# Kernel optimization log

Hardware: AMD Instinct MI355X
Metric: run time of the kernel (lower is better)

Reference implementation:

```python
import jax, jax.numpy as jnp
import numpy as np

B, C, H, W = 4, 256, 64, 64
G = 32          # GroupNorm groups
EPS = 1e-6


def setup_inputs() -> dict:
    key = jax.random.key(0)
    ks = jax.random.split(key, 6)
    inp = {
        "x": jax.random.normal(ks[0], (B, C, H, W), dtype=jnp.float32),
        "gamma": jnp.ones((C,), jnp.float32),
        "beta": jnp.zeros((C,), jnp.float32),
        "wq": jax.random.normal(ks[1], (C, C), jnp.float32) * 0.02,
        "bq": jnp.zeros((C,), jnp.float32),
        "wk": jax.random.normal(ks[2], (C, C), jnp.float32) * 0.02,
        "bk": jnp.zeros((C,), jnp.float32),
        "wv": jax.random.normal(ks[3], (C, C), jnp.float32) * 0.02,
        "bv": jnp.zeros((C,), jnp.float32),
        "wp": jax.random.normal(ks[4], (C, C), jnp.float32) * 0.02,
        "bp": jnp.zeros((C,), jnp.float32),
    }
    return inp


def _group_norm(x, gamma, beta):
    b, c, h, w = x.shape
    xs = x.reshape(b, G, c // G, h, w)
    mu = xs.mean(axis=(2, 3, 4), keepdims=True)
    var = xs.var(axis=(2, 3, 4), keepdims=True)  # biased, matches torch GroupNorm
    xn = ((xs - mu) * jax.lax.rsqrt(var + EPS)).reshape(b, c, h, w)
    return xn * gamma[None, :, None, None] + beta[None, :, None, None]


def _conv1x1(s, w, bias):
    # 1x1 conv == per-pixel channel matmul
    return jnp.einsum('oc,bchw->bohw', w, s) + bias[None, :, None, None]


def reference(x, gamma, beta, wq, bq, wk, bk, wv, bv, wp, bp):
    b, c, h, w = x.shape
    s = _group_norm(x, gamma, beta)
    q = _conv1x1(s, wq, bq).reshape(b, c, h * w)  # [B, C, N]
    k = _conv1x1(s, wk, bk).reshape(b, c, h * w)
    v = _conv1x1(s, wv, bv).reshape(b, c, h * w)
    # scores[b,i,j] = sum_c q[b,c,i] k[b,c,j], scaled by C^-1/2
    scores = jnp.einsum('bci,bcj->bij', q, k) * (c ** -0.5)
    attn = jax.nn.softmax(scores, axis=2)
    # h_[b,c,i] = sum_j v[b,c,j] attn[b,i,j]
    h_ = jnp.einsum('bij,bcj->bci', attn, v).reshape(b, c, h, w)
    h_ = _conv1x1(h_, wp, bp)
    return x + h_
```

## Files before the change

kernel.cpp:

```cpp
#include <hip/hip_runtime.h>

#define BB 4
#define CCH 256
#define NPIX 4096
#define EPS 1e-6f

typedef __attribute__((ext_vector_type(8))) short bf16x8;
typedef __attribute__((ext_vector_type(4))) float f32x4;
typedef __attribute__((ext_vector_type(16))) float f32x16;

__device__ __forceinline__ unsigned short f2bf(float f) {
    return (unsigned short)((__float_as_uint(f) + 0x8000u) >> 16);
}
__device__ __forceinline__ float bf2f(unsigned short h) {
    return __uint_as_float((unsigned)h << 16);
}
__device__ __forceinline__ void gl2lds16(const void* g, void* l) {
    __builtin_amdgcn_global_load_lds(
        (const __attribute__((address_space(1))) unsigned int*)g,
        (__attribute__((address_space(3))) unsigned int*)l, 16, 0, 0);
}

__global__ __launch_bounds__(256) void gn_apply(const float* __restrict__ x,
                                                const float* __restrict__ gamma,
                                                const float* __restrict__ beta,
                                                unsigned short* __restrict__ sb) {
    int bg = blockIdx.x;
    int b = bg >> 5, g = bg & 31;
    const float4* x4 = (const float4*)(x + (size_t)(b * CCH + g * 8) * NPIX);
    float s = 0.f, ss = 0.f;
    for (int e = threadIdx.x; e < 8 * NPIX / 4; e += 256) {
        float4 v = x4[e];
        s += v.x + v.y + v.z + v.w;
        ss += v.x * v.x + v.y * v.y + v.z * v.z + v.w * v.w;
    }
    __shared__ float rs[256], rss[256];
    __shared__ float mean_s, rstd_s;
    rs[threadIdx.x] = s; rss[threadIdx.x] = ss;
    __syncthreads();
    for (int off = 128; off > 0; off >>= 1) {
        if (threadIdx.x < (unsigned)off) {
            rs[threadIdx.x] += rs[threadIdx.x + off];
            rss[threadIdx.x] += rss[threadIdx.x + off];
        }
        __syncthreads();
    }
    if (threadIdx.x == 0) {
        const float inv = 1.0f / (float)(8 * NPIX);
        float m = rs[0] * inv;
        float var = rss[0] * inv - m * m;
        mean_s = m;
        rstd_s = rsqrtf(var + EPS);
    }
    __syncthreads();
    float scale[8], shift[8];
#pragma unroll
    for (int ci = 0; ci < 8; ++ci) {
        float ga = gamma[g * 8 + ci], be = beta[g * 8 + ci];
        scale[ci] = rstd_s * ga;
        shift[ci] = be - mean_s * scale[ci];
    }
#pragma unroll 1
    for (int r = 0; r < 4; ++r) {
        int pq = r * 256 + threadIdx.x;
        __align__(16) unsigned short h[4][8];
#pragma unroll
        for (int ci = 0; ci < 8; ++ci) {
            float4 v = x4[ci * 1024 + pq];
            h[0][ci] = f2bf(v.x * scale[ci] + shift[ci]);
            h[1][ci] = f2bf(v.y * scale[ci] + shift[ci]);
            h[2][ci] = f2bf(v.z * scale[ci] + shift[ci]);
            h[3][ci] = f2bf(v.w * scale[ci] + shift[ci]);
        }
        size_t base = ((size_t)(b * NPIX + pq * 4) << 8) + g * 8;
#pragma unroll
        for (int p = 0; p < 4; ++p)
            *(uint4*)(sb + base + (size_t)p * 256) = *(const uint4*)h[p];
    }
}

__global__ __launch_bounds__(256) void wcvt(const float* __restrict__ wq,
                                            const float* __restrict__ wk,
                                            const float* __restrict__ wv,
                                            const float* __restrict__ wp,
                                            unsigned short* __restrict__ wb) {
    int e = blockIdx.x * 256 + threadIdx.x;
    const float* srcs[4] = {wp, wq, wk, wv};
#pragma unroll
    for (int m = 0; m < 4; ++m) {
        float4 v = ((const float4*)srcs[m])[e];
        ushort4 h;
        h.x = f2bf(v.x); h.y = f2bf(v.y); h.z = f2bf(v.z); h.w = f2bf(v.w);
        *(ushort4*)(wb + (size_t)m * 65536 + (size_t)e * 4) = h;
    }
}

__global__ __launch_bounds__(256) void qkv_mfma(
    const unsigned short* __restrict__ sb, const unsigned short* __restrict__ wb,
    const float* __restrict__ bq, const float* __restrict__ bk,
    const float* __restrict__ bv,
    unsigned short* __restrict__ qT, unsigned short* __restrict__ kT,
    unsigned short* __restrict__ vB) {
    __shared__ __align__(16) char lds[34816];
    const int tid = threadIdx.x, lane = tid & 63, w = tid >> 6;
    const int ln15 = lane & 15, q = lane >> 4;
    const int n0 = blockIdx.x * 128;
    const int co0 = blockIdx.y * 128;
    const int z = blockIdx.z;
    const unsigned short* wm = wb + (size_t)(z + 1) * 65536;
    const float* bias = (z == 0) ? bq : (z == 1) ? bk : bv;

    f32x4 acc[2][8];
#pragma unroll
    for (int i2 = 0; i2 < 2; ++i2)
#pragma unroll
        for (int nf = 0; nf < 8; ++nf) {
            acc[i2][nf][0] = 0.f; acc[i2][nf][1] = 0.f;
            acc[i2][nf][2] = 0.f; acc[i2][nf][3] = 0.f;
        }

#pragma unroll 1
    for (int kt = 0; kt < 4; ++kt) {
#pragma unroll
        for (int r = 0; r < 4; ++r) {
            int gch = r * 256 + tid;
            int row = gch >> 3, sidx = gch & 7;
            int cc = sidx ^ (row & 7);
            gl2lds16(sb + ((size_t)(n0 + row) << 8) + kt * 64 + cc * 8,
                     &lds[r * 4096 + w * 1024]);
            gl2lds16(wm + ((size_t)(co0 + row) << 8) + kt * 64 + cc * 8,
                     &lds[16384 + r * 4096 + w * 1024]);
        }
        __syncthreads();
#pragma unroll
        for (int kk = 0; kk < 2; ++kk) {
            int kc = kk * 4 + q;
            bf16x8 af[2], bf[8];
#pragma unroll
            for (int i2 = 0; i2 < 2; ++i2) {
                int row = w * 32 + i2 * 16 + ln15;
                af[i2] = *(const bf16x8*)&lds[row * 128 + ((kc ^ (row & 7)) << 4)];
            }
#pragma unroll
            for (int nf = 0; nf < 8; ++nf) {
                int row = nf * 16 + ln15;
                bf[nf] = *(const bf16x8*)&lds[16384 + row * 128 + ((kc ^ (row & 7)) << 4)];
            }
#pragma unroll
            for (int i2 = 0; i2 < 2; ++i2)
#pragma unroll
                for (int nf = 0; nf < 8; ++nf)
                    acc[i2][nf] = __builtin_amdgcn_mfma_f32_16x16x32_bf16(
                        af[i2], bf[nf], acc[i2][nf], 0, 0, 0);
        }
        __syncthreads();
    }

    float bias_l[8];
#pragma unroll
    for (int nf = 0; nf < 8; ++nf) bias_l[nf] = bias[co0 + nf * 16 + ln15];
    const float scl = (z == 0) ? 0.0625f : 1.0f;
    unsigned short* T = (unsigned short*)lds;
    if (z < 2) {
#pragma unroll
        for (int i2 = 0; i2 < 2; ++i2)
#pragma unroll
            for (int nf = 0; nf < 8; ++nf)
#pragma unroll
                for (int r = 0; r < 4; ++r) {
                    int n_l = w * 32 + i2 * 16 + q * 4 + r;
                    int co_l = nf * 16 + ln15;
                    T[n_l * 136 + co_l] = f2bf((acc[i2][nf][r] + bias_l[nf]) * scl);
                }
    } else {
#pragma unroll
        for (int i2 = 0; i2 < 2; ++i2)
#pragma unroll
            for (int nf = 0; nf < 8; ++nf)
#pragma unroll
                for (int r = 0; r < 4; ++r) {
                    int n_l = w * 32 + i2 * 16 + q * 4 + r;
                    int co_l = nf * 16 + ln15;
                    T[co_l * 136 + n_l] = f2bf(acc[i2][nf][r] + bias_l[nf]);
                }
    }
    __syncthreads();
    int row = tid >> 1, half = tid & 1;
    const uint4* src = (const uint4*)&T[row * 136 + half * 64];
    uint4* dst;
    if (z < 2) {
        unsigned short* qk = (z == 0) ? qT : kT;
        dst = (uint4*)(qk + ((size_t)(n0 + row) << 8) + co0 + half * 64);
    } else {
        int b2 = n0 >> 12, pix0 = n0 & 4095;
        dst = (uint4*)(vB + ((size_t)(b2 * CCH + co0 + row) << 12) + pix0 + half * 64);
    }
#pragma unroll
    for (int u = 0; u < 8; ++u) dst[u] = src[u];
}

__global__ __launch_bounds__(512, 2) void attn_mfma(
    const unsigned short* __restrict__ qT, const unsigned short* __restrict__ kT,
    const unsigned short* __restrict__ vB,
    unsigned short* __restrict__ pO, float* __restrict__ pml) {
    __shared__ __align__(16) char lds[81920];
    const int tid = threadIdx.x, lane = tid & 63, w = tid >> 6;
    const int l31 = lane & 31, lh = lane >> 5;
    const int bx = blockIdx.x;
    const int xk = bx & 7;
    const int b = xk >> 1, jqhi = xk & 1;
    const int outer = bx >> 3;
    const int jqlo = outer & 1, itile = outer >> 1;
    const int i0 = itile * 128;
    const int jbase = (jqhi * 2 + jqlo) * 1024;
    const size_t nb = (size_t)b * NPIX;
    const int iqb = (w >> 1) * 32;
    const int jh = w & 1, jwb = jh * 32;
    const int ipb = (w & 1) * 64;
    const int cqb = (w >> 1) * 64;

#pragma unroll
    for (int t = 0; t < 8; ++t) {
        int gch = (w * 8 + t) * 64 + lane;
        int row = gch >> 5, sc = gch & 31;
        int cc = sc ^ (row & 7);
        gl2lds16(qT + ((nb + i0 + row) << 8) + cc * 8, &lds[(w * 8 + t) * 1024]);
    }
    __syncthreads();
    bf16x8 qf[16];
    {
        int row = iqb + l31;
#pragma unroll
        for (int kc = 0; kc < 16; ++kc) {
            int sc = kc * 2 + lh;
            qf[kc] = *(const bf16x8*)&lds[row * 512 + ((sc ^ (row & 7)) << 4)];
        }
    }
    __syncthreads();

    f32x16 O[2][2];
#pragma unroll
    for (int ig = 0; ig < 2; ++ig)
#pragma unroll
        for (int cg = 0; cg < 2; ++cg)
#pragma unroll
            for (int r = 0; r < 16; ++r) O[ig][cg][r] = 0.f;
    float l_acc[16];
#pragma unroll
    for (int r = 0; r < 16; ++r) l_acc[r] = 0.f;

    {
        const int j0 = jbase;
#pragma unroll
        for (int t = 0; t < 4; ++t) {
            int gch = (w * 4 + t) * 64 + lane;
            int row = gch >> 5, sc = gch & 31;
            int cc = sc ^ (row & 7);
            gl2lds16(kT + ((nb + j0 + row) << 8) + cc * 8, &lds[(w * 4 + t) * 1024]);
        }
#pragma unroll
        for (int t = 0; t < 4; ++t) {
            int gch = (w * 4 + t) * 64 + lane;
            int c = gch >> 3, sv = gch & 7;
            int jc = sv ^ (c & 7);
            gl2lds16(vB + ((size_t)(b * CCH + c) << 12) + j0 + jc * 8,
                     &lds[32768 + (w * 4 + t) * 1024]);
        }
    }

#pragma unroll 1
    for (int jt = 0; jt < 16; ++jt) {
        asm volatile("s_waitcnt vmcnt(4)" ::: "memory");
        __builtin_amdgcn_s_barrier();

        f32x16 S0, S1;
#pragma unroll
        for (int r = 0; r < 16; ++r) { S0[r] = 0.f; S1[r] = 0.f; }
        __builtin_amdgcn_s_setprio(1);
        {
            int krow = jwb + l31;
            int ksw = krow * 512;
#pragma unroll
            for (int kc = 0; kc < 8; ++kc) {
                int sc0 = (2 * kc) * 2 + lh;
                int sc1 = (2 * kc + 1) * 2 + lh;
                bf16x8 k0 = *(const bf16x8*)&lds[ksw + ((sc0 ^ (krow & 7)) << 4)];
                bf16x8 k1 = *(const bf16x8*)&lds[ksw + ((sc1 ^ (krow & 7)) << 4)];
                S0 = __builtin_amdgcn_mfma_f32_32x32x16_bf16(qf[2 * kc], k0, S0, 0, 0, 0);
                S1 = __builtin_amdgcn_mfma_f32_32x32x16_bf16(qf[2 * kc + 1], k1, S1, 0, 0, 0);
            }
        }
        __builtin_amdgcn_s_setprio(0);

        asm volatile("" ::: "memory");
        __builtin_amdgcn_s_barrier();
        if (jt < 15) {
            const int j0n = jbase + (jt + 1) * 64;
#pragma unroll
            for (int t = 0; t < 4; ++t) {
                int gch = (w * 4 + t) * 64 + lane;
                int row = gch >> 5, sc = gch & 31;
                int cc = sc ^ (row & 7);
                gl2lds16(kT + ((nb + j0n + row) << 8) + cc * 8,
                         &lds[(w * 4 + t) * 1024]);
            }
        }

        {
            int col = jwb + l31;
            int chs = (col >> 3) << 4;
            int cof = (col & 7) << 1;
#pragma unroll
            for (int r = 0; r < 16; ++r) {
                float p = __expf(S0[r] + S1[r]);
                l_acc[r] += p;
                int row = iqb + (r & 3) + 8 * (r >> 2) + 4 * lh;
                *(unsigned short*)&lds[65536 + row * 128 +
                    (chs ^ ((row & 7) << 4)) + cof] = f2bf(p);
            }
        }
        asm volatile("s_waitcnt lgkmcnt(0)" ::: "memory");
        __builtin_amdgcn_sched_barrier(0);

        if (jt < 15) {
            asm volatile("s_waitcnt vmcnt(4)" ::: "memory");
        } else {
            asm volatile("s_waitcnt vmcnt(0)" ::: "memory");
        }
        __builtin_amdgcn_s_barrier();

        __builtin_amdgcn_s_setprio(1);
        {
            int pr0 = ipb + l31, pr1 = ipb + 32 + l31;
            int vc0 = cqb + l31, vc1 = cqb + 32 + l31;
#pragma unroll
            for (int kc = 0; kc < 4; ++kc) {
                int pc = kc * 2 + lh;
                bf16x8 pf0 = *(const bf16x8*)&lds[65536 + pr0 * 128 + ((pc ^ (pr0 & 7)) << 4)];
                bf16x8 pf1 = *(const bf16x8*)&lds[65536 + pr1 * 128 + ((pc ^ (pr1 & 7)) << 4)];
                bf16x8 vf0 = *(const bf16x8*)&lds[32768 + vc0 * 128 + ((pc ^ (vc0 & 7)) << 4)];
                bf16x8 vf1 = *(const bf16x8*)&lds[32768 + vc1 * 128 + ((pc ^ (vc1 & 7)) << 4)];
                O[0][0] = __builtin_amdgcn_mfma_f32_32x32x16_bf16(pf0, vf0, O[0][0], 0, 0, 0);
                O[0][1] = __builtin_amdgcn_mfma_f32_32x32x16_bf16(pf0, vf1, O[0][1], 0, 0, 0);
                O[1][0] = __builtin_amdgcn_mfma_f32_32x32x16_bf16(pf1, vf0, O[1][0], 0, 0, 0);
                O[1][1] = __builtin_amdgcn_mfma_f32_32x32x16_bf16(pf1, vf1, O[1][1], 0, 0, 0);
            }
        }
        __builtin_amdgcn_s_setprio(0);

        asm volatile("" ::: "memory");
        __builtin_amdgcn_s_barrier();
        if (jt < 15) {
            const int j0n = jbase + (jt + 1) * 64;
#pragma unroll
            for (int t = 0; t < 4; ++t) {
                int gch = (w * 4 + t) * 64 + lane;
                int c = gch >> 3, sv = gch & 7;
                int jc = sv ^ (c & 7);
                gl2lds16(vB + ((size_t)(b * CCH + c) << 12) + j0n + jc * 8,
                         &lds[32768 + (w * 4 + t) * 1024]);
            }
        }
    }

    size_t pbase = (size_t)bx * (128 * 256);
#pragma unroll
    for (int ig = 0; ig < 2; ++ig)
#pragma unroll
        for (int cg = 0; cg < 2; ++cg)
#pragma unroll
            for (int r = 0; r < 16; ++r) {
                int i = ipb + ig * 32 + (r & 3) + 8 * (r >> 2) + 4 * lh;
                int c = cqb + cg * 32 + l31;
                pO[pbase + i * 256 + c] = f2bf(O[ig][cg][r]);
            }
#pragma unroll
    for (int r = 0; r < 16; ++r) {
        float l = l_acc[r];
        l += __shfl_xor(l, 1);
        l += __shfl_xor(l, 2);
        l += __shfl_xor(l, 4);
        l += __shfl_xor(l, 8);
        l += __shfl_xor(l, 16);
        if (l31 == 0) {
            int row = iqb + (r & 3) + 8 * (r >> 2) + 4 * lh;
            pml[bx * 256 + jh * 128 + row] = l;
        }
    }
}

__global__ __launch_bounds__(256) void attn_merge(
    const unsigned short* __restrict__ pO, const float* __restrict__ pml,
    unsigned short* __restrict__ hN) {
    int bid = blockIdx.x;
    int b = bid & 3, itile = (bid >> 2) & 31, ih = (bid >> 7) & 1;
    int base = itile * 16 + b * 2;
    const int offs[4] = {0, 1, 8, 9};
    __shared__ float fs[64];
    int t = threadIdx.x;
    if (t < 64) {
        float l = 0.f;
#pragma unroll
        for (int s = 0; s < 4; ++s) {
            int px = (base + offs[s]) * 256 + ih * 64 + t;
            l += pml[px] + pml[px + 128];
        }
        fs[t] = 1.0f / l;
    }
    __syncthreads();
    int i = t >> 2, cq = t & 3;
    float f = fs[i];
    int row = ih * 64 + i;
    size_t nrow = ((size_t)(b * NPIX + itile * 128 + row)) << 8;
#pragma unroll
    for (int p = 0; p < 16; ++p) {
        int c = p * 16 + cq * 4;
        float o0 = 0.f, o1 = 0.f, o2 = 0.f, o3 = 0.f;
#pragma unroll
        for (int s = 0; s < 4; ++s) {
            ushort4 a = *(const ushort4*)&pO[(size_t)(base + offs[s]) * 32768 + row * 256 + c];
            o0 += bf2f(a.x); o1 += bf2f(a.y); o2 += bf2f(a.z); o3 += bf2f(a.w);
        }
        ushort4 h;
        h.x = f2bf(o0 * f); h.y = f2bf(o1 * f);
        h.z = f2bf(o2 * f); h.w = f2bf(o3 * f);
        *(ushort4*)&hN[nrow + c] = h;
    }
}

__global__ __launch_bounds__(256) void proj_mfma(
    const unsigned short* __restrict__ hN, const unsigned short* __restrict__ wb,
    const float* __restrict__ bp, const float* __restrict__ x,
    float* __restrict__ out) {
    __shared__ __align__(16) char lds[34816];
    const int tid = threadIdx.x, lane = tid & 63, w = tid >> 6;
    const int ln15 = lane & 15, q = lane >> 4;
    const int n0 = blockIdx.x * 128;
    const int co0 = blockIdx.y * 128;

    f32x4 acc[2][8];
#pragma unroll
    for (int i2 = 0; i2 < 2; ++i2)
#pragma unroll
        for (int nf = 0; nf < 8; ++nf) {
            acc[i2][nf][0] = 0.f; acc[i2][nf][1] = 0.f;
            acc[i2][nf][2] = 0.f; acc[i2][nf][3] = 0.f;
        }

#pragma unroll 1
    for (int kt = 0; kt < 4; ++kt) {
#pragma unroll
        for (int r = 0; r < 4; ++r) {
            int gch = r * 256 + tid;
            int row = gch >> 3, sidx = gch & 7;
            int cc = sidx ^ (row & 7);
            gl2lds16(hN + ((size_t)(n0 + row) << 8) + kt * 64 + cc * 8,
                     &lds[r * 4096 + w * 1024]);
            gl2lds16(wb + ((size_t)(co0 + row) << 8) + kt * 64 + cc * 8,
                     &lds[16384 + r * 4096 + w * 1024]);
        }
        __syncthreads();
#pragma unroll
        for (int kk = 0; kk < 2; ++kk) {
            int kc = kk * 4 + q;
            bf16x8 af[2], bf[8];
#pragma unroll
            for (int i2 = 0; i2 < 2; ++i2) {
                int row = w * 32 + i2 * 16 + ln15;
                af[i2] = *(const bf16x8*)&lds[row * 128 + ((kc ^ (row & 7)) << 4)];
            }
#pragma unroll
            for (int nf = 0; nf < 8; ++nf) {
                int row = nf * 16 + ln15;
                bf[nf] = *(const bf16x8*)&lds[16384 + row * 128 + ((kc ^ (row & 7)) << 4)];
            }
#pragma unroll
            for (int i2 = 0; i2 < 2; ++i2)
#pragma unroll
                for (int nf = 0; nf < 8; ++nf)
                    acc[i2][nf] = __builtin_amdgcn_mfma_f32_16x16x32_bf16(
                        af[i2], bf[nf], acc[i2][nf], 0, 0, 0);
        }
        __syncthreads();
    }

    unsigned short* T = (unsigned short*)lds;
#pragma unroll
    for (int i2 = 0; i2 < 2; ++i2)
#pragma unroll
        for (int nf = 0; nf < 8; ++nf)
#pragma unroll
            for (int r = 0; r < 4; ++r) {
                int n_l = w * 32 + i2 * 16 + q * 4 + r;
                int co_l = nf * 16 + ln15;
                T[co_l * 136 + n_l] = f2bf(acc[i2][nf][r]);
            }
    __syncthreads();
    int row = tid >> 1, half = tid & 1;
    int b2 = n0 >> 12, pix0 = n0 & 4095;
    float br = bp[co0 + row];
    size_t gidx = (((size_t)(b2 * CCH + co0 + row)) << 12) + pix0 + half * 64;
    const unsigned short* trow = &T[row * 136 + half * 64];
#pragma unroll
    for (int u = 0; u < 16; ++u) {
        float4 xv = *(const float4*)&x[gidx + u * 4];
        ushort4 tv = *(const ushort4*)&trow[u * 4];
        float4 o;
        o.x = xv.x + br + bf2f(tv.x);
        o.y = xv.y + br + bf2f(tv.y);
        o.z = xv.z + br + bf2f(tv.z);
        o.w = xv.w + br + bf2f(tv.w);
        *(float4*)&out[gidx + u * 4] = o;
    }
}

extern "C" void kernel_launch(void* const* d_in, const int* in_sizes, int n_in,
                              void* d_out, int out_size, void* d_ws, size_t ws_size,
                              hipStream_t stream) {
    const float* x     = (const float*)d_in[0];
    const float* gamma = (const float*)d_in[1];
    const float* beta  = (const float*)d_in[2];
    const float* wq    = (const float*)d_in[3];
    const float* bq    = (const float*)d_in[4];
    const float* wk    = (const float*)d_in[5];
    const float* bk    = (const float*)d_in[6];
    const float* wv    = (const float*)d_in[7];
    const float* bv    = (const float*)d_in[8];
    const float* wp    = (const float*)d_in[9];
    const float* bp    = (const float*)d_in[10];
    float* out = (float*)d_out;

    char* p = (char*)d_ws;
    unsigned short* sb  = (unsigned short*)p; p += 8388608;
    unsigned short* hN  = sb;
    unsigned short* wb  = (unsigned short*)p; p += 524288;
    unsigned short* pO  = (unsigned short*)p; p += 33554432;
    float*          pml = (float*)p;          p += 524288;
    unsigned short* qT  = (unsigned short*)p; p += 8388608;
    unsigned short* kT  = (unsigned short*)p; p += 8388608;
    unsigned short* vB  = (unsigned short*)p;

    gn_apply<<<BB * 32, 256, 0, stream>>>(x, gamma, beta, sb);
    wcvt<<<64, 256, 0, stream>>>(wq, wk, wv, wp, wb);
    qkv_mfma<<<dim3(128, 2, 3), 256, 0, stream>>>(sb, wb, bq, bk, bv, qT, kT, vB);
    attn_mfma<<<512, 512, 0, stream>>>(qT, kT, vB, pO, pml);
    attn_merge<<<256, 256, 0, stream>>>(pO, pml, hN);
    proj_mfma<<<dim3(128, 2), 256, 0, stream>>>(hN, wb, bp, x, out);
}
```

Baseline: 236.6 us.

## Split GroupNorm into stats and normalize kernels, fold weight conversion into stats

The single GroupNorm kernel, which ran only 128 blocks, becomes two kernels. The first computes partial sums over half a group in each of 256 blocks, and 64 extra blocks in the same launch convert the weights to bf16. The second launch combines the two partials per group and writes normalized bf16 activations across 256 blocks. The aim is better occupancy of the GPU's many CUs for the memory-bound normalization. The cost is reading x twice from separate launches, which may come from cache, plus a small partial-stats buffer; the launch count stays the same.

```diff
diff --git a/kernel.cpp b/kernel.cpp
--- a/kernel.cpp
+++ b/kernel.cpp
@@ -21,77 +21,83 @@
         (__attribute__((address_space(3))) unsigned int*)l, 16, 0, 0);
 }
 
-__global__ __launch_bounds__(256) void gn_apply(const float* __restrict__ x,
-                                                const float* __restrict__ gamma,
-                                                const float* __restrict__ beta,
-                                                unsigned short* __restrict__ sb) {
-    int bg = blockIdx.x;
-    int b = bg >> 5, g = bg & 31;
+__global__ __launch_bounds__(256) void gn_stats(
+    const float* __restrict__ x, float2* __restrict__ pst,
+    const float* __restrict__ wq, const float* __restrict__ wk,
+    const float* __restrict__ wv, const float* __restrict__ wp,
+    unsigned short* __restrict__ wb) {
+    int bid = blockIdx.x;
+    int t = threadIdx.x;
+    if (bid >= 256) {
+        int e = (bid - 256) * 256 + t;
+        const float* srcs[4] = {wp, wq, wk, wv};
+#pragma unroll
+        for (int m = 0; m < 4; ++m) {
+            float4 v = ((const float4*)srcs[m])[e];
+            ushort4 hh;
+            hh.x = f2bf(v.x); hh.y = f2bf(v.y);
+            hh.z = f2bf(v.z); hh.w = f2bf(v.w);
+            *(ushort4*)(wb + (size_t)m * 65536 + (size_t)e * 4) = hh;
+        }
+        return;
+    }
+    int b = bid >> 6, g = (bid >> 1) & 31, h = bid & 1;
     const float4* x4 = (const float4*)(x + (size_t)(b * CCH + g * 8) * NPIX);
     float s = 0.f, ss = 0.f;
-    for (int e = threadIdx.x; e < 8 * NPIX / 4; e += 256) {
+    for (int e = h * 4096 + t; e < h * 4096 + 4096; e += 256) {
         float4 v = x4[e];
         s += v.x + v.y + v.z + v.w;
         ss += v.x * v.x + v.y * v.y + v.z * v.z + v.w * v.w;
     }
     __shared__ float rs[256], rss[256];
-    __shared__ float mean_s, rstd_s;
-    rs[threadIdx.x] = s; rss[threadIdx.x] = ss;
+    rs[t] = s; rss[t] = ss;
     __syncthreads();
     for (int off = 128; off > 0; off >>= 1) {
-        if (threadIdx.x < (unsigned)off) {
-            rs[threadIdx.x] += rs[threadIdx.x + off];
-            rss[threadIdx.x] += rss[threadIdx.x + off];
+        if (t < (unsigned)off) {
+            rs[t] += rs[t + off];
+            rss[t] += rss[t + off];
         }
         __syncthreads();
     }
-    if (threadIdx.x == 0) {
-        const float inv = 1.0f / (float)(8 * NPIX);
-        float m = rs[0] * inv;
-        float var = rss[0] * inv - m * m;
-        mean_s = m;
-        rstd_s = rsqrtf(var + EPS);
-    }
-    __syncthreads();
+    if (t == 0) pst[bid] = make_float2(rs[0], rss[0]);
+}
+
+__global__ __launch_bounds__(256) void gn_norm(
+    const float* __restrict__ x, const float2* __restrict__ pst,
+    const float* __restrict__ gamma, const float* __restrict__ beta,
+    unsigned short* __restrict__ sb) {
+    int bid = blockIdx.x;
+    int b = bid >> 6, g = (bid >> 1) & 31, h = bid & 1;
+    float2 p0 = pst[bid & ~1];
+    float2 p1 = pst[bid | 1];
+    const float inv = 1.0f / (float)(8 * NPIX);
+    float m = (p0.x + p1.x) * inv;
+    float var = (p0.y + p1.y) * inv - m * m;
+    float rstd = rsqrtf(var + EPS);
     float scale[8], shift[8];
 #pragma unroll
     for (int ci = 0; ci < 8; ++ci) {
         float ga = gamma[g * 8 + ci], be = beta[g * 8 + ci];
-        scale[ci] = rstd_s * ga;
-        shift[ci] = be - mean_s * scale[ci];
-    }
+        scale[ci] = rstd * ga;
+        shift[ci] = be - m * scale[ci];
+    }
+    const float4* x4 = (const float4*)(x + (size_t)(b * CCH + g * 8) * NPIX);
 #pragma unroll 1
-    for (int r = 0; r < 4; ++r) {
-        int pq = r * 256 + threadIdx.x;
-        __align__(16) unsigned short h[4][8];
+    for (int r = 0; r < 2; ++r) {
+        int pq = h * 512 + r * 256 + threadIdx.x;
+        __align__(16) unsigned short hh[4][8];
 #pragma unroll
         for (int ci = 0; ci < 8; ++ci) {
             float4 v = x4[ci * 1024 + pq];
-            h[0][ci] = f2bf(v.x * scale[ci] + shift[ci]);
-            h[1][ci] = f2bf(v.y * scale[ci] + shift[ci]);
-            h[2][ci] = f2bf(v.z * scale[ci] + shift[ci]);
-            h[3][ci] = f2bf(v.w * scale[ci] + shift[ci]);
+            hh[0][ci] = f2bf(v.x * scale[ci] + shift[ci]);
+            hh[1][ci] = f2bf(v.y * scale[ci] + shift[ci]);
+            hh[2][ci] = f2bf(v.z * scale[ci] + shift[ci]);
+            hh[3][ci] = f2bf(v.w * scale[ci] + shift[ci]);
         }
         size_t base = ((size_t)(b * NPIX + pq * 4) << 8) + g * 8;
 #pragma unroll
         for (int p = 0; p < 4; ++p)
-            *(uint4*)(sb + base + (size_t)p * 256) = *(const uint4*)h[p];
-    }
-}
-
-__global__ __launch_bounds__(256) void wcvt(const float* __restrict__ wq,
-                                            const float* __restrict__ wk,
-                                            const float* __restrict__ wv,
-                                            const float* __restrict__ wp,
-                                            unsigned short* __restrict__ wb) {
-    int e = blockIdx.x * 256 + threadIdx.x;
-    const float* srcs[4] = {wp, wq, wk, wv};
-#pragma unroll
-    for (int m = 0; m < 4; ++m) {
-        float4 v = ((const float4*)srcs[m])[e];
-        ushort4 h;
-        h.x = f2bf(v.x); h.y = f2bf(v.y); h.z = f2bf(v.z); h.w = f2bf(v.w);
-        *(ushort4*)(wb + (size_t)m * 65536 + (size_t)e * 4) = h;
+            *(uint4*)(sb + base + (size_t)p * 256) = *(const uint4*)hh[p];
     }
 }
 
@@ -536,12 +542,13 @@
     unsigned short* wb  = (unsigned short*)p; p += 524288;
     unsigned short* pO  = (unsigned short*)p; p += 33554432;
     float*          pml = (float*)p;          p += 524288;
+    float2*         pst = (float2*)p;         p += 4096;
     unsigned short* qT  = (unsigned short*)p; p += 8388608;
     unsigned short* kT  = (unsigned short*)p; p += 8388608;
     unsigned short* vB  = (unsigned short*)p;
 
-    gn_apply<<<BB * 32, 256, 0, stream>>>(x, gamma, beta, sb);
-    wcvt<<<64, 256, 0, stream>>>(wq, wk, wv, wp, wb);
+    gn_stats<<<320, 256, 0, stream>>>(x, pst, wq, wk, wv, wp, wb);
+    gn_norm<<<256, 256, 0, stream>>>(x, pst, gamma, beta, sb);
     qkv_mfma<<<dim3(128, 2, 3), 256, 0, stream>>>(sb, wb, bq, bk, bv, qT, kT, vB);
     attn_mfma<<<512, 512, 0, stream>>>(qT, kT, vB, pO, pml);
     attn_merge<<<256, 256, 0, stream>>>(pO, pml, hN);
```

Measured after the change: 230.3 us. 1.03x faster.
